# Kernel optimization log

Hardware: AMD Instinct MI355X
Metric: run time of the kernel (lower is better)

The kernel has to match this reference:

```python
import jax, jax.numpy as jnp
import numpy as np

NGRAM = 16
SUB = 512  # bytes per sub-block


def byte2image(block, ngram=NGRAM):
    """block: (B, L) int -> (B, 1, ngram*8, L-ngram) float32 in [-1, 1]."""
    B, L = block.shape
    blk = block.astype(jnp.int32)
    # nxt[:, i] = blk[:, i+1], last column zero
    nxt = jnp.concatenate([blk[:, 1:], jnp.zeros((B, 1), jnp.int32)], axis=1)
    # 8 bit-shifted views of the byte stream
    shifts = jnp.stack(
        [((blk << s) & 255) + ((nxt >> (8 - s)) & 255) for s in range(8)],
        axis=1,
    )  # (B, 8, L)
    flat = shifts.reshape(B, -1)  # (B, 8*L)
    parts = [flat] + [jnp.roll(flat, -i, axis=1) for i in range(1, ngram)]
    stacked = jnp.concatenate(parts, axis=1).reshape(B, ngram * 8, L)
    result = stacked[:, :, :-ngram].astype(jnp.float32)
    result = (result / 255.0 - 0.5) / 0.5
    return result[:, None]  # (B, 1, ngram*8, L-ngram)


def byte2image_4k(block, ngram=NGRAM):
    """block: (B, 4096) -> (B, 8, ngram*8, 512-ngram)."""
    return jnp.concatenate(
        [byte2image(block[:, i * SUB:(i + 1) * SUB], ngram) for i in range(8)],
        axis=1,
    )


def setup_inputs() -> dict:
    key = jax.random.key(0)
    kx, kw = jax.random.split(key)
    x = jax.random.randint(kx, (256, 4096), 0, 256, dtype=jnp.int64)
    W = jax.random.normal(kw, (496, 64), dtype=jnp.float32) * 0.02
    return {"x": x, "W": W}


def reference(x, W):
    # ByteFormerWrapper.forward with block_size=4096: byte2image_4k then the
    # (opaque) model; model stood in by a linear head over the image width.
    img = byte2image_4k(x)                      # (B, 8, 128, 496)
    out = jnp.einsum('bchw,wo->bcho', img, W)   # (B, 8, 128, 64)
    return out
```

## Files before the change

kernel.cpp:

```cpp
#include <hip/hip_runtime.h>

typedef unsigned short u16;
typedef unsigned int u32;
typedef _Float16 half8 __attribute__((ext_vector_type(8)));
typedef __fp16 fp16x2 __attribute__((ext_vector_type(2)));
typedef __attribute__((ext_vector_type(4))) float floatx4;

#define LSTRIDE 72

__device__ __forceinline__ u32 pkrtz(float lo, float hi) {
  fp16x2 h = __builtin_amdgcn_cvt_pkrtz(lo, hi);
  return __builtin_bit_cast(u32, h);
}

__global__ __launch_bounds__(256, 3) void byteformer_fused(
    const int* __restrict__ x, const float* __restrict__ Wm,
    float* __restrict__ out) {
  __shared__ __align__(16) u16 As[128 * LSTRIDE];
  __shared__ __align__(16) u16 Bs[128 * LSTRIDE];
  __shared__ float part[256];
  __shared__ float csum[64];

  const int t = threadIdx.x;
  const int mtile = blockIdx.x;
  const int n0 = blockIdx.y * 128;
  const int p0 = 2 * blockIdx.y;

  const int wave = t >> 6, lane = t & 63;
  const int wm = wave >> 1, wn = wave & 1;
  const int quad = lane >> 4, l16 = lane & 15;

  const int sA_sub = t >> 4;
  const int sA_kg  = (t >> 1) & 7;
  const int sA_qh  = t & 1;
  const long xrow = ((long)mtile * 16 + sA_sub) * 512;
  const int sB_o = lane;

  floatx4 acc[4][4];
  #pragma unroll
  for (int mt = 0; mt < 4; ++mt)
    #pragma unroll
    for (int nt = 0; nt < 4; ++nt)
      acc[mt][nt] = floatx4{0.f, 0.f, 0.f, 0.f};

  float csum_local = 0.0f;

  int4 a0, a1; int c8; float f[17];

  auto loadG = [&](int kc, int4& A0, int4& A1, int& C8, float (&F)[17]) {
    const int base = kc * 64 + sA_kg * 8;
    A0 = *(const int4*)&x[xrow + base];
    A1 = *(const int4*)&x[xrow + base + 4];
    C8 = (base + 8 < 512) ? x[xrow + base + 8] : 0;
    const int cb = kc * 64 + 16 * wave - p0 - 1;
    #pragma unroll
    for (int j = 0; j < 17; ++j) {
      int c = cb + j;
      F[j] = (c >= 0 && c < 496) ? Wm[c * 64 + sB_o] : 0.0f;
    }
  };

  auto writeLDS = [&]() {
    int c[9] = {a0.x, a0.y, a0.z, a0.w, a1.x, a1.y, a1.z, a1.w, c8};
    u32 w16[8];
    #pragma unroll
    for (int j = 0; j < 8; ++j) w16[j] = ((u32)c[j] << 8) | (u32)c[j + 1];
    #pragma unroll
    for (int qi = 0; qi < 4; ++qi) {
      const int q = sA_qh * 4 + qi;
      const int sh = 8 - q;
      u32 d[4];
      #pragma unroll
      for (int jp = 0; jp < 4; ++jp) {
        u32 v0 = (w16[2 * jp] >> sh) & 255u;
        u32 v1 = (w16[2 * jp + 1] >> sh) & 255u;
        d[jp] = v0 | (v1 << 16) | 0x64006400u;
      }
      *(uint4*)&As[(sA_sub * 8 + q) * LSTRIDE + sA_kg * 8] =
          uint4{d[0], d[1], d[2], d[3]};
    }
    u32 pe[8], po[8];
    #pragma unroll
    for (int i = 0; i < 8; ++i) {
      pe[i] = pkrtz(f[2 * i], f[2 * i + 1]);
      po[i] = pkrtz(f[2 * i + 1], f[2 * i + 2]);
    }
    #pragma unroll
    for (int g = 0; g < 2; ++g) {
      const int mgrp = 2 * wave + g;
      *(uint4*)&Bs[(0 * 64 + sB_o) * LSTRIDE + mgrp * 8] =
          uint4{po[g * 4], po[g * 4 + 1], po[g * 4 + 2], po[g * 4 + 3]};
      *(uint4*)&Bs[(1 * 64 + sB_o) * LSTRIDE + mgrp * 8] =
          uint4{pe[g * 4], pe[g * 4 + 1], pe[g * 4 + 2], pe[g * 4 + 3]};
    }
    #pragma unroll
    for (int j = 1; j <= 16; ++j) csum_local += f[j];
  };

  loadG(0, a0, a1, c8, f);
  writeLDS();
  __syncthreads();

  for (int kc = 0; kc < 8; ++kc) {
    int4 na0, na1; int nc8; float nf[17];
    if (kc < 7) loadG(kc + 1, na0, na1, nc8, nf);

    #pragma unroll
    for (int ks = 0; ks < 2; ++ks) {
      const int koff = ks * 32 + quad * 8;
      half8 af[4], bf[4];
      #pragma unroll
      for (int mt = 0; mt < 4; ++mt)
        af[mt] = *(const half8*)&As[(wm * 64 + mt * 16 + l16) * LSTRIDE + koff];
      #pragma unroll
      for (int nt = 0; nt < 4; ++nt)
        bf[nt] = *(const half8*)&Bs[(wn * 64 + nt * 16 + l16) * LSTRIDE + koff];
      #pragma unroll
      for (int mt = 0; mt < 4; ++mt)
        #pragma unroll
        for (int nt = 0; nt < 4; ++nt)
          acc[mt][nt] = __builtin_amdgcn_mfma_f32_16x16x32_f16(
              af[mt], bf[nt], acc[mt][nt], 0, 0, 0);
    }
    __syncthreads();
    if (kc < 7) {
      a0 = na0; a1 = na1; c8 = nc8;
      #pragma unroll
      for (int j = 0; j < 17; ++j) f[j] = nf[j];
      writeLDS();
      __syncthreads();
    }
  }

  part[t] = csum_local;
  __syncthreads();
  if (t < 64)
    csum[t] = part[t] + part[t + 64] + part[t + 128] + part[t + 192];
  __syncthreads();

  const float S = 2.0f / 255.0f;
  const float K1 = 1024.0f * S + 1.0f;
  const int p = p0 + wn;
  float cs[4];
  #pragma unroll
  for (int nt = 0; nt < 4; ++nt) cs[nt] = K1 * csum[nt * 16 + l16];
  #pragma unroll
  for (int mt = 0; mt < 4; ++mt) {
    int mbase = mtile * 128 + wm * 64 + mt * 16 + quad * 4;
    #pragma unroll
    for (int i = 0; i < 4; ++i) {
      int mr = mbase + i;
      int bid = mr >> 3, q = mr & 7;
      float* orow = out + (long)bid * 8192 + (p * 8 + q) * 64;
      #pragma unroll
      for (int nt = 0; nt < 4; ++nt)
        orow[nt * 16 + l16] = S * acc[mt][nt][i] - cs[nt];
    }
  }
}

extern "C" void kernel_launch(void* const* d_in, const int* in_sizes, int n_in,
                              void* d_out, int out_size, void* d_ws, size_t ws_size,
                              hipStream_t stream) {
  const int* x = (const int*)d_in[0];
  const float* Wm = (const float*)d_in[1];
  float* out = (float*)d_out;
  byteformer_fused<<<dim3(128, 8), dim3(256), 0, stream>>>(x, Wm, out);
}
```

Measured before the change: 105.3 us.

## Precompute shifted fp16 weight matrix in a prep kernel and widen GEMM N-tile

Splits the fused kernel into a prep kernel and a GEMM kernel. The prep kernel builds a pre-scaled, shifted fp16 copy of W for every phase offset, plus the column sums, and writes both to workspace. The GEMM kernel then streams the B tiles straight from global memory into LDS with a double-buffered register prefetch, instead of converting W and reducing its sums inside every block. It also doubles the N tile to 256, with 4x8 MFMA accumulators per wave and occupancy lowered to 2, so each A tile is reused more. The cost is an extra kernel launch and higher register pressure.

```diff
diff --git a/kernel.cpp b/kernel.cpp
--- a/kernel.cpp
+++ b/kernel.cpp
@@ -13,55 +13,82 @@
   return __builtin_bit_cast(u32, h);
 }
 
-__global__ __launch_bounds__(256, 3) void byteformer_fused(
-    const int* __restrict__ x, const float* __restrict__ Wm,
-    float* __restrict__ out) {
+__global__ __launch_bounds__(256) void prep_kernel(const float* __restrict__ Wm,
+                                                   u16* __restrict__ Btg,
+                                                   float* __restrict__ csum_g) {
+  const int b = blockIdx.x, t = threadIdx.x;
+  if (b < 256) {
+    int gid = b * 256 + t;
+    int o = gid & 63;
+    int m8 = (gid >> 6) & 63;
+    int p = gid >> 12;
+    const float S = 2.0f / 255.0f;
+    float f[8];
+    #pragma unroll
+    for (int j = 0; j < 8; ++j) {
+      int c = m8 * 8 + j - p;
+      f[j] = (c >= 0 && c < 496) ? Wm[c * 64 + o] * S : 0.0f;
+    }
+    uint4 d = uint4{pkrtz(f[0], f[1]), pkrtz(f[2], f[3]),
+                    pkrtz(f[4], f[5]), pkrtz(f[6], f[7])};
+    *(uint4*)&Btg[(p * 64 + o) * 512 + m8 * 8] = d;
+  } else {
+    __shared__ float red[256];
+    int o = t & 63, seg = t >> 6;
+    float s = 0.0f;
+    for (int c = seg; c < 496; c += 4) s += Wm[c * 64 + o];
+    red[t] = s;
+    __syncthreads();
+    if (t < 64) csum_g[t] = red[t] + red[t + 64] + red[t + 128] + red[t + 192];
+  }
+}
+
+struct Regs {
+  int4 a0, a1; int c8;
+  uint4 b[8];
+};
+
+__global__ __launch_bounds__(256, 2) void gemm_kernel(
+    const int* __restrict__ x, const u16* __restrict__ Btg,
+    const float* __restrict__ csum_g, float* __restrict__ out) {
   __shared__ __align__(16) u16 As[128 * LSTRIDE];
-  __shared__ __align__(16) u16 Bs[128 * LSTRIDE];
-  __shared__ float part[256];
-  __shared__ float csum[64];
+  __shared__ __align__(16) u16 Bs[256 * LSTRIDE];
 
   const int t = threadIdx.x;
   const int mtile = blockIdx.x;
-  const int n0 = blockIdx.y * 128;
-  const int p0 = 2 * blockIdx.y;
+  const int n0 = blockIdx.y * 256;
 
   const int wave = t >> 6, lane = t & 63;
   const int wm = wave >> 1, wn = wave & 1;
   const int quad = lane >> 4, l16 = lane & 15;
 
-  const int sA_sub = t >> 4;
-  const int sA_kg  = (t >> 1) & 7;
-  const int sA_qh  = t & 1;
+  const int sA_sub = t >> 4, sA_kg = (t >> 1) & 7, sA_qh = t & 1;
   const long xrow = ((long)mtile * 16 + sA_sub) * 512;
-  const int sB_o = lane;
+  const int sB_row = t >> 3, sB_kg = t & 7;
 
-  floatx4 acc[4][4];
+  floatx4 acc[4][8];
   #pragma unroll
   for (int mt = 0; mt < 4; ++mt)
     #pragma unroll
-    for (int nt = 0; nt < 4; ++nt)
+    for (int nt = 0; nt < 8; ++nt)
       acc[mt][nt] = floatx4{0.f, 0.f, 0.f, 0.f};
 
-  float csum_local = 0.0f;
+  Regs r[2];
 
-  int4 a0, a1; int c8; float f[17];
-
-  auto loadG = [&](int kc, int4& A0, int4& A1, int& C8, float (&F)[17]) {
+  auto loadG = [&](int kc, Regs& R) {
     const int base = kc * 64 + sA_kg * 8;
-    A0 = *(const int4*)&x[xrow + base];
-    A1 = *(const int4*)&x[xrow + base + 4];
-    C8 = (base + 8 < 512) ? x[xrow + base + 8] : 0;
-    const int cb = kc * 64 + 16 * wave - p0 - 1;
+    R.a0 = *(const int4*)&x[xrow + base];
+    R.a1 = *(const int4*)&x[xrow + base + 4];
+    R.c8 = (base + 8 < 512) ? x[xrow + base + 8] : 0;
+    const long bbase = (long)(n0 + sB_row) * 512 + kc * 64 + sB_kg * 8;
     #pragma unroll
-    for (int j = 0; j < 17; ++j) {
-      int c = cb + j;
-      F[j] = (c >= 0 && c < 496) ? Wm[c * 64 + sB_o] : 0.0f;
-    }
+    for (int pass = 0; pass < 8; ++pass)
+      R.b[pass] = *(const uint4*)&Btg[bbase + (long)pass * (32 * 512)];
   };
 
-  auto writeLDS = [&]() {
-    int c[9] = {a0.x, a0.y, a0.z, a0.w, a1.x, a1.y, a1.z, a1.w, c8};
+  auto writeLDS = [&](Regs& R) {
+    int c[9] = {R.a0.x, R.a0.y, R.a0.z, R.a0.w,
+                R.a1.x, R.a1.y, R.a1.z, R.a1.w, R.c8};
     u32 w16[8];
     #pragma unroll
     for (int j = 0; j < 8; ++j) w16[j] = ((u32)c[j] << 8) | (u32)c[j + 1];
@@ -79,71 +106,49 @@
       *(uint4*)&As[(sA_sub * 8 + q) * LSTRIDE + sA_kg * 8] =
           uint4{d[0], d[1], d[2], d[3]};
     }
-    u32 pe[8], po[8];
     #pragma unroll
-    for (int i = 0; i < 8; ++i) {
-      pe[i] = pkrtz(f[2 * i], f[2 * i + 1]);
-      po[i] = pkrtz(f[2 * i + 1], f[2 * i + 2]);
-    }
-    #pragma unroll
-    for (int g = 0; g < 2; ++g) {
-      const int mgrp = 2 * wave + g;
-      *(uint4*)&Bs[(0 * 64 + sB_o) * LSTRIDE + mgrp * 8] =
-          uint4{po[g * 4], po[g * 4 + 1], po[g * 4 + 2], po[g * 4 + 3]};
-      *(uint4*)&Bs[(1 * 64 + sB_o) * LSTRIDE + mgrp * 8] =
-          uint4{pe[g * 4], pe[g * 4 + 1], pe[g * 4 + 2], pe[g * 4 + 3]};
-    }
-    #pragma unroll
-    for (int j = 1; j <= 16; ++j) csum_local += f[j];
+    for (int pass = 0; pass < 8; ++pass)
+      *(uint4*)&Bs[(sB_row + 32 * pass) * LSTRIDE + sB_kg * 8] = R.b[pass];
   };
 
-  loadG(0, a0, a1, c8, f);
-  writeLDS();
+  loadG(0, r[0]);
+  writeLDS(r[0]);
   __syncthreads();
 
+  #pragma unroll
   for (int kc = 0; kc < 8; ++kc) {
-    int4 na0, na1; int nc8; float nf[17];
-    if (kc < 7) loadG(kc + 1, na0, na1, nc8, nf);
+    if (kc < 7) loadG(kc + 1, r[(kc + 1) & 1]);
 
     #pragma unroll
     for (int ks = 0; ks < 2; ++ks) {
       const int koff = ks * 32 + quad * 8;
-      half8 af[4], bf[4];
+      half8 af[4], bf[8];
       #pragma unroll
       for (int mt = 0; mt < 4; ++mt)
         af[mt] = *(const half8*)&As[(wm * 64 + mt * 16 + l16) * LSTRIDE + koff];
       #pragma unroll
-      for (int nt = 0; nt < 4; ++nt)
-        bf[nt] = *(const half8*)&Bs[(wn * 64 + nt * 16 + l16) * LSTRIDE + koff];
+      for (int nt = 0; nt < 8; ++nt)
+        bf[nt] = *(const half8*)&Bs[(wn * 128 + nt * 16 + l16) * LSTRIDE + koff];
       #pragma unroll
       for (int mt = 0; mt < 4; ++mt)
         #pragma unroll
-        for (int nt = 0; nt < 4; ++nt)
+        for (int nt = 0; nt < 8; ++nt)
           acc[mt][nt] = __builtin_amdgcn_mfma_f32_16x16x32_f16(
               af[mt], bf[nt], acc[mt][nt], 0, 0, 0);
     }
     __syncthreads();
     if (kc < 7) {
-      a0 = na0; a1 = na1; c8 = nc8;
-      #pragma unroll
-      for (int j = 0; j < 17; ++j) f[j] = nf[j];
-      writeLDS();
+      writeLDS(r[(kc + 1) & 1]);
       __syncthreads();
     }
   }
 
-  part[t] = csum_local;
-  __syncthreads();
-  if (t < 64)
-    csum[t] = part[t] + part[t + 64] + part[t + 128] + part[t + 192];
-  __syncthreads();
-
   const float S = 2.0f / 255.0f;
   const float K1 = 1024.0f * S + 1.0f;
-  const int p = p0 + wn;
   float cs[4];
   #pragma unroll
-  for (int nt = 0; nt < 4; ++nt) cs[nt] = K1 * csum[nt * 16 + l16];
+  for (int j = 0; j < 4; ++j) cs[j] = K1 * csum_g[j * 16 + l16];
+  const int pbase = (n0 + wn * 128) >> 6;
   #pragma unroll
   for (int mt = 0; mt < 4; ++mt) {
     int mbase = mtile * 128 + wm * 64 + mt * 16 + quad * 4;
@@ -151,10 +156,13 @@
     for (int i = 0; i < 4; ++i) {
       int mr = mbase + i;
       int bid = mr >> 3, q = mr & 7;
-      float* orow = out + (long)bid * 8192 + (p * 8 + q) * 64;
+      float* ob = out + (long)bid * 8192 + q * 64;
       #pragma unroll
-      for (int nt = 0; nt < 4; ++nt)
-        orow[nt * 16 + l16] = S * acc[mt][nt][i] - cs[nt];
+      for (int nt = 0; nt < 8; ++nt) {
+        int p = pbase + (nt >> 2);
+        int o = (nt & 3) * 16 + l16;
+        ob[(long)p * 512 + o] = acc[mt][nt][i] - cs[nt & 3];
+      }
     }
   }
 }
@@ -165,5 +173,10 @@
   const int* x = (const int*)d_in[0];
   const float* Wm = (const float*)d_in[1];
   float* out = (float*)d_out;
-  byteformer_fused<<<dim3(128, 8), dim3(256), 0, stream>>>(x, Wm, out);
+
+  u16* Btg = (u16*)d_ws;
+  float* csum_g = (float*)((char*)d_ws + (1u << 20));
+
+  prep_kernel<<<dim3(257), dim3(256), 0, stream>>>(Wm, Btg, csum_g);
+  gemm_kernel<<<dim3(128, 4), dim3(256), 0, stream>>>(x, Btg, csum_g, out);
 }
```

Measured after the change: 145.5 us. 1.38x slower.
